# Optimization experiments

Measured on AMD Instinct MI355X. Metric: run time of the kernel, lower is better.

## Reference

```python
import jax, jax.numpy as jnp
import numpy as np

N_NODES = 50000
N_EDGES = 200000
D = 128
LN_EPS = 1e-5


def _layer_norm(x, g, b):
    mu = jnp.mean(x, axis=-1, keepdims=True)
    var = jnp.mean(jnp.square(x - mu), axis=-1, keepdims=True)
    return (x - mu) * jax.lax.rsqrt(var + LN_EPS) * g + b


def _mlp(x, W1, b1, W2, b2, W3, b3, g, beta):
    # 2 hidden ReLU layers + linear output + LayerNorm (MeshGraphNets style)
    h = jax.nn.relu(x @ W1 + b1)
    h = jax.nn.relu(h @ W2 + b2)
    h = h @ W3 + b3
    return _layer_norm(h, g, beta)


def setup_inputs() -> dict:
    key = jax.random.key(0)
    ks = jax.random.split(key, 12)
    d = {}
    d["node_features"] = jax.random.normal(ks[0], (N_NODES, D), dtype=jnp.float32)
    d["edge_features"] = jax.random.normal(ks[1], (N_EDGES, D), dtype=jnp.float32)
    d["senders"] = jax.random.randint(ks[2], (N_EDGES,), 0, N_NODES, dtype=jnp.int32)
    d["receivers"] = jax.random.randint(ks[3], (N_EDGES,), 0, N_NODES, dtype=jnp.int32)
    def lin(k, fan_in, fan_out):
        return jax.random.normal(k, (fan_in, fan_out), dtype=jnp.float32) / np.sqrt(fan_in)
    # edge MLP: [3D] -> D -> D -> D
    d["We1"] = lin(ks[4], 3 * D, D); d["be1"] = jnp.zeros((D,), jnp.float32)
    d["We2"] = lin(ks[5], D, D);     d["be2"] = jnp.zeros((D,), jnp.float32)
    d["We3"] = lin(ks[6], D, D);     d["be3"] = jnp.zeros((D,), jnp.float32)
    d["ge"] = jnp.ones((D,), jnp.float32); d["bege"] = jnp.zeros((D,), jnp.float32)
    # node MLP: [2D] -> D -> D -> D
    d["Wn1"] = lin(ks[7], 2 * D, D); d["bn1"] = jnp.zeros((D,), jnp.float32)
    d["Wn2"] = lin(ks[8], D, D);     d["bn2"] = jnp.zeros((D,), jnp.float32)
    d["Wn3"] = lin(ks[9], D, D);     d["bn3"] = jnp.zeros((D,), jnp.float32)
    d["gn"] = jnp.ones((D,), jnp.float32); d["begn"] = jnp.zeros((D,), jnp.float32)
    return d


def reference(node_features, edge_features, senders, receivers,
              We1, be1, We2, be2, We3, be3, ge, bege,
              Wn1, bn1, Wn2, bn2, Wn3, bn3, gn, begn):
    num_nodes = node_features.shape[0]
    # --- edge update: gather sender/receiver feats, concat, edge MLP ---
    edge_in = jnp.concatenate(
        [node_features[senders], node_features[receivers], edge_features], axis=-1)  # [E, 3D]
    new_edge = _mlp(edge_in, We1, be1, We2, be2, We3, be3, ge, bege)  # [E, D]
    # --- node update: scatter-sum aggregate, concat, node MLP ---
    agg = jax.ops.segment_sum(new_edge, receivers, num_segments=num_nodes)  # [N, D]
    node_in = jnp.concatenate([node_features, agg], axis=-1)  # [N, 2D]
    new_node = _mlp(node_in, Wn1, bn1, Wn2, bn2, Wn3, bn3, gn, begn)
    # --- residuals ---
    new_node = new_node + node_features
    new_edge = new_edge + edge_features
    return new_node, new_edge
```

## Files before the change

kernel.cpp:

```cpp
#include <hip/hip_runtime.h>

#define NNODES 50000
#define NEDGES 200000
#define DD 128
#define LN_EPS 1e-5f
#define NTH 256

typedef __attribute__((ext_vector_type(8))) short bf16x8;
typedef __attribute__((ext_vector_type(4))) float f32x4;
typedef __attribute__((ext_vector_type(16))) float f32x16;

template<int N> struct ic { static constexpr int value = N; };

__device__ __forceinline__ unsigned short bf_rne(float f) {
    union { float f; unsigned u; } v; v.f = f;
    return (unsigned short)((v.u + 0x7fffu + ((v.u >> 16) & 1u)) >> 16);
}

__device__ __forceinline__ void gload_lds16(const void* g, void* l) {
    __builtin_amdgcn_global_load_lds(
        (const __attribute__((address_space(1))) void*)g,
        (__attribute__((address_space(3))) void*)l, 16, 0, 0);
}

__global__ void build_wimg(const float* __restrict__ We1, const float* __restrict__ We2,
                           const float* __restrict__ We3, const float* __restrict__ Wn1,
                           const float* __restrict__ Wn2, const float* __restrict__ Wn3,
                           char* __restrict__ img_e, char* __restrict__ img_n) {
    int tid = blockIdx.x * NTH + threadIdx.x;
    const float* W; char* dst; int q;
    if      (tid <  6144) { W = We1; dst = img_e;             q = tid;         }
    else if (tid <  8192) { W = We2; dst = img_e + 12 * 8192; q = tid - 6144;  }
    else if (tid < 10240) { W = We3; dst = img_e + 16 * 8192; q = tid - 8192;  }
    else if (tid < 14336) { W = Wn1; dst = img_n;             q = tid - 10240; }
    else if (tid < 16384) { W = Wn2; dst = img_n + 8 * 8192;  q = tid - 14336; }
    else if (tid < 18432) { W = Wn3; dst = img_n + 12 * 8192; q = tid - 16384; }
    else return;
    int c = q >> 9, rem = q & 511;
    int ntile = rem >> 7, r2 = rem & 127, n32 = r2 >> 2, ks = r2 & 3;
    int n = ntile * 32 + n32;
    int sx = (n32 + (n32 >> 2)) & 3;
    int k0 = c * 32 + ks * 8;
    unsigned short o[8];
    #pragma unroll
    for (int e = 0; e < 8; ++e)
        o[e] = bf_rne(W[(size_t)(k0 + e) * DD + n]);
    uint4 val;
    val.x = (unsigned)o[0] | ((unsigned)o[1] << 16);
    val.y = (unsigned)o[2] | ((unsigned)o[3] << 16);
    val.z = (unsigned)o[4] | ((unsigned)o[5] << 16);
    val.w = (unsigned)o[6] | ((unsigned)o[7] << 16);
    *(uint4*)(dst + (size_t)c * 8192 + ntile * 2048 + n32 * 64 + ((ks ^ sx) << 4)) = val;
}

__global__ void csr_histo(const int* __restrict__ recv, int* __restrict__ cnt) {
    int e = blockIdx.x * NTH + threadIdx.x;
    if (e < NEDGES) atomicAdd(&cnt[recv[e]], 1);
}

__global__ __launch_bounds__(1024)
void csr_scan(const int* __restrict__ cnt, int* __restrict__ off, int* __restrict__ cursor) {
    __shared__ int part[1024];
    const int t = threadIdx.x;
    const int CH = (NNODES + 1023) / 1024;
    const int base = t * CH;
    int s = 0;
    for (int i = 0; i < CH; ++i) {
        int idx = base + i;
        if (idx < NNODES) s += cnt[idx];
    }
    part[t] = s;
    __syncthreads();
    for (int d = 1; d < 1024; d <<= 1) {
        int v = (t >= d) ? part[t - d] : 0;
        __syncthreads();
        part[t] += v;
        __syncthreads();
    }
    int run = (t == 0) ? 0 : part[t - 1];
    for (int i = 0; i < CH; ++i) {
        int idx = base + i;
        if (idx < NNODES) {
            off[idx] = run; cursor[idx] = run;
            run += cnt[idx];
        }
    }
    if (t == 1023) off[NNODES] = NEDGES;
}

__global__ void csr_fill(const int* __restrict__ recv, int* __restrict__ cursor,
                         int* __restrict__ elist) {
    int e = blockIdx.x * NTH + threadIdx.x;
    if (e < NEDGES) {
        int p = atomicAdd(&cursor[recv[e]], 1);
        elist[p] = e;
    }
}

__global__ __launch_bounds__(NTH)
void aggregate(const float* __restrict__ oute, const float* __restrict__ edgef,
               const int* __restrict__ off, const int* __restrict__ elist,
               float* __restrict__ agg) {
    const int n = blockIdx.x * 4 + (threadIdx.x >> 6);
    const int l = threadIdx.x & 63;
    if (n >= NNODES) return;
    const int j0 = off[n], j1 = off[n + 1];
    float ax = 0.f, ay = 0.f, bx = 0.f, by = 0.f;
    int j = j0;
    for (; j + 1 < j1; j += 2) {
        const int e0 = elist[j], e1 = elist[j + 1];
        const float2 o0 = ((const float2*)(oute  + (size_t)e0 * DD))[l];
        const float2 f0 = ((const float2*)(edgef + (size_t)e0 * DD))[l];
        const float2 o1 = ((const float2*)(oute  + (size_t)e1 * DD))[l];
        const float2 f1 = ((const float2*)(edgef + (size_t)e1 * DD))[l];
        ax += o0.x - f0.x; ay += o0.y - f0.y;
        bx += o1.x - f1.x; by += o1.y - f1.y;
    }
    if (j < j1) {
        const int e = elist[j];
        const float2 o  = ((const float2*)(oute  + (size_t)e * DD))[l];
        const float2 ef = ((const float2*)(edgef + (size_t)e * DD))[l];
        ax += o.x - ef.x; ay += o.y - ef.y;
    }
    float2 r; r.x = ax + bx; r.y = ay + by;
    ((float2*)(agg + (size_t)n * DD))[l] = r;
}

template<int MODE>
__global__ __launch_bounds__(NTH, 2)
void mgn_mfma(const float* __restrict__ nodef, const float* __restrict__ edgef,
              const int* __restrict__ senders, const int* __restrict__ receivers,
              const char* __restrict__ img,
              const float* __restrict__ b1, const float* __restrict__ b2,
              const float* __restrict__ b3,
              const float* __restrict__ gamma, const float* __restrict__ beta,
              const float* __restrict__ agg, float* __restrict__ outp)
{
    __shared__ char Wbuf[5 * 8192];
    __shared__ char Hb[4 * 8192];

    const int t  = threadIdx.x;
    const int w  = t >> 6;
    const int l  = t & 63;
    const int ln = l & 31;
    const int hi = l >> 5;
    const int row0 = blockIdx.x * 128;
    const int gm = row0 + w * 32 + ln;
    constexpr int NROWS = (MODE == 0) ? NEDGES : NNODES;
    constexpr int NK1   = (MODE == 0) ? 12 : 8;
    constexpr int NCH   = NK1 + 8;
    const int gmc = gm < NROWS ? gm : NROWS - 1;
    const int sxA = (ln + (ln >> 2)) & 3;
    const int sxH = ln & 15;

    int srow = 0, rrow = 0;
    if (MODE == 0) { srow = senders[gmc]; rrow = receivers[gmc]; }

    const f32x16 fz = {0.f,0.f,0.f,0.f,0.f,0.f,0.f,0.f,
                       0.f,0.f,0.f,0.f,0.f,0.f,0.f,0.f};
    f32x16 acc[4];
    #pragma unroll
    for (int nt = 0; nt < 4; ++nt) acc[nt] = fz;

    f32x4 barr[3][4];

    auto stageW = [&](int c) {
        const char* src = img + (size_t)c * 8192 + t * 16;
        char* dstl = Wbuf + (c % 5) * 8192 + t * 16;
        gload_lds16(src, dstl);
        gload_lds16(src + 4096, dstl + 4096);
    };

    auto loadBG = [&](int c, f32x4* dst) {
        const float* base;
        if (MODE == 0) {
            base = (c < 4) ? nodef + (size_t)srow * DD
                 : (c < 8) ? nodef + (size_t)rrow * DD
                           : edgef + (size_t)gmc * DD;
        } else {
            base = (c < 4) ? nodef + (size_t)gmc * DD
                           : agg   + (size_t)gmc * DD;
        }
        const float* p = base + (c & 3) * 32 + hi * 8;
        dst[0] = *(const f32x4*)p;
        dst[1] = *(const f32x4*)(p + 4);
        dst[2] = *(const f32x4*)(p + 16);
        dst[3] = *(const f32x4*)(p + 20);
    };

    auto cvtB = [&](const f32x4* br) {
        bf16x8 r;
        #pragma unroll
        for (int i = 0; i < 4; ++i) r[i]     = (short)bf_rne(br[0][i]);
        #pragma unroll
        for (int i = 0; i < 4; ++i) r[4 + i] = (short)bf_rne(br[1][i]);
        return r;
    };

    auto loadBH = [&](int ks, int kh) {
        const char* p = Hb + w * 8192 + ln * 256
                      + (((ks * 4 + kh * 2 + hi) ^ sxH) << 4);
        return *(const bf16x8*)p;
    };

    auto epiH = [&](const float* bias) {
        #pragma unroll
        for (int nt = 0; nt < 4; ++nt) {
            #pragma unroll
            for (int rq = 0; rq < 4; ++rq) {
                f32x4 bv = *(const f32x4*)(bias + nt * 32 + rq * 8 + hi * 4);
                unsigned short h[4];
                #pragma unroll
                for (int j = 0; j < 4; ++j)
                    h[j] = bf_rne(fmaxf(acc[nt][rq * 4 + j] + bv[j], 0.f));
                char* p = Hb + w * 8192 + ln * 256
                        + (((nt * 4 + rq) ^ sxH) << 4) + hi * 8;
                unsigned lo = (unsigned)h[0] | ((unsigned)h[1] << 16);
                unsigned hx = (unsigned)h[2] | ((unsigned)h[3] << 16);
                *(unsigned long long*)p =
                    (unsigned long long)lo | ((unsigned long long)hx << 32);
            }
            acc[nt] = fz;
        }
    };

    auto compute = [&](auto cc) {
        constexpr int c = decltype(cc)::value;
        const char* bp = Wbuf + (c % 5) * 8192 + ln * 64;
        #pragma unroll
        for (int kh = 0; kh < 2; ++kh) {
            bf16x8 b;
            if constexpr (c < NK1) b = cvtB(&barr[c % 3][kh * 2]);
            else                   b = loadBH((c - NK1) & 3, kh);
            #pragma unroll
            for (int nt = 0; nt < 4; ++nt) {
                bf16x8 a = *(const bf16x8*)(bp + nt * 2048
                            + (((kh * 2 + hi) ^ sxA) << 4));
                acc[nt] = __builtin_amdgcn_mfma_f32_32x32x16_bf16(a, b, acc[nt], 0, 0, 0);
            }
        }
    };

#define PITER(C, VM)                                                        \
    {                                                                       \
        if constexpr ((C) + 3 < NCH) stageW((C) + 3);                       \
        __builtin_amdgcn_sched_barrier(0);                                  \
        if constexpr ((C) + 2 < NK1) loadBG((C) + 2, barr[((C) + 2) % 3]);  \
        __builtin_amdgcn_sched_barrier(0);                                  \
        asm volatile("s_waitcnt vmcnt(" #VM ")" ::: "memory");              \
        __builtin_amdgcn_sched_barrier(0);                                  \
        __builtin_amdgcn_s_barrier();                                       \
        __builtin_amdgcn_sched_barrier(0);                                  \
        compute(ic<(C)>{});                                                 \
    }

    stageW(0);
    __builtin_amdgcn_sched_barrier(0);
    loadBG(0, barr[0]);
    __builtin_amdgcn_sched_barrier(0);
    stageW(1);
    __builtin_amdgcn_sched_barrier(0);
    loadBG(1, barr[1]);
    __builtin_amdgcn_sched_barrier(0);
    stageW(2);
    __builtin_amdgcn_sched_barrier(0);

    if constexpr (MODE == 0) {
        PITER(0, 18)  PITER(1, 18)  PITER(2, 18)  PITER(3, 22)  PITER(4, 22)
        PITER(5, 22)  PITER(6, 22)  PITER(7, 22)  PITER(8, 22)  PITER(9, 22)
        PITER(10, 18) PITER(11, 14)
        epiH(b1);
        PITER(12, 10) PITER(13, 6)  PITER(14, 6)  PITER(15, 6)
        epiH(b2);
        PITER(16, 6)  PITER(17, 4)  PITER(18, 2)  PITER(19, 0)
    } else {
        PITER(0, 18)  PITER(1, 18)  PITER(2, 18)  PITER(3, 22)  PITER(4, 22)
        PITER(5, 22)  PITER(6, 18)  PITER(7, 14)
        epiH(b1);
        PITER(8, 10)  PITER(9, 6)   PITER(10, 6)  PITER(11, 6)
        epiH(b2);
        PITER(12, 6)  PITER(13, 4)  PITER(14, 2)  PITER(15, 0)
    }
#undef PITER

    float vsum = 0.f, vsq = 0.f;
    #pragma unroll
    for (int nt = 0; nt < 4; ++nt) {
        #pragma unroll
        for (int rq = 0; rq < 4; ++rq) {
            f32x4 bv = *(const f32x4*)(b3 + nt * 32 + rq * 8 + hi * 4);
            #pragma unroll
            for (int j = 0; j < 4; ++j) {
                float v = acc[nt][rq * 4 + j] + bv[j];
                acc[nt][rq * 4 + j] = v;
                vsum += v; vsq += v * v;
            }
        }
    }
    vsum += __shfl_xor(vsum, 32);
    vsq  += __shfl_xor(vsq, 32);
    const float mu = vsum * (1.f / DD);
    const float rs = rsqrtf(vsq * (1.f / DD) - mu * mu + LN_EPS);

    if (gm < NROWS) {
        const float* resid = ((MODE == 0) ? edgef : nodef) + (size_t)gm * DD;
        #pragma unroll
        for (int nt = 0; nt < 4; ++nt) {
            #pragma unroll
            for (int rq = 0; rq < 4; ++rq) {
                const int n0 = nt * 32 + rq * 8 + hi * 4;
                f32x4 gv = *(const f32x4*)(gamma + n0);
                f32x4 bv = *(const f32x4*)(beta + n0);
                f32x4 rv = *(const f32x4*)(resid + n0);
                f32x4 o;
                #pragma unroll
                for (int j = 0; j < 4; ++j)
                    o[j] = (acc[nt][rq * 4 + j] - mu) * rs * gv[j] + bv[j] + rv[j];
                *(f32x4*)(outp + (size_t)gm * DD + n0) = o;
            }
        }
    }
}

extern "C" void kernel_launch(void* const* d_in, const int* in_sizes, int n_in,
                              void* d_out, int out_size, void* d_ws, size_t ws_size,
                              hipStream_t stream) {
    const float* nodef = (const float*)d_in[0];
    const float* edgef = (const float*)d_in[1];
    const int* senders   = (const int*)d_in[2];
    const int* receivers = (const int*)d_in[3];
    const float* We1 = (const float*)d_in[4],  *be1 = (const float*)d_in[5];
    const float* We2 = (const float*)d_in[6],  *be2 = (const float*)d_in[7];
    const float* We3 = (const float*)d_in[8],  *be3 = (const float*)d_in[9];
    const float* ge  = (const float*)d_in[10], *bege = (const float*)d_in[11];
    const float* Wn1 = (const float*)d_in[12], *bn1 = (const float*)d_in[13];
    const float* Wn2 = (const float*)d_in[14], *bn2 = (const float*)d_in[15];
    const float* Wn3 = (const float*)d_in[16], *bn3 = (const float*)d_in[17];
    const float* gn  = (const float*)d_in[18], *begn = (const float*)d_in[19];

    float* out_node = (float*)d_out;
    float* out_edge = (float*)d_out + (size_t)NNODES * DD;

    char* ws = (char*)d_ws;
    size_t o = 0;
    float* agg  = (float*)(ws + o); o += (size_t)NNODES * DD * 4;
    char* img_e = ws + o;           o += 20 * 8192;
    char* img_n = ws + o;           o += 16 * 8192;
    int* cnt    = (int*)(ws + o);   o += NNODES * 4;
    int* cursor = (int*)(ws + o);   o += NNODES * 4;
    int* off    = (int*)(ws + o);   o += (NNODES + 4) * 4;
    int* elist  = (int*)(ws + o);   o += NEDGES * 4;

    hipMemsetAsync(cnt, 0, NNODES * 4, stream);
    build_wimg<<<72, NTH, 0, stream>>>(We1, We2, We3, Wn1, Wn2, Wn3, img_e, img_n);

    const int egrid = (NEDGES + NTH - 1) / NTH;
    csr_histo<<<egrid, NTH, 0, stream>>>(receivers, cnt);
    csr_scan<<<1, 1024, 0, stream>>>(cnt, off, cursor);
    csr_fill<<<egrid, NTH, 0, stream>>>(receivers, cursor, elist);

    mgn_mfma<0><<<dim3((NEDGES + 127) / 128), dim3(NTH), 0, stream>>>(
        nodef, edgef, senders, receivers, img_e,
        be1, be2, be3, ge, bege, agg, out_edge);

    aggregate<<<(NNODES + 3) / 4, NTH, 0, stream>>>(out_edge, edgef, off, elist, agg);

    mgn_mfma<1><<<dim3((NNODES + 127) / 128), dim3(NTH), 0, stream>>>(
        nodef, edgef, senders, receivers, img_n,
        bn1, bn2, bn3, gn, begn, agg, out_node);
}
```

Baseline: 329.2 us.

## Load weights from global into registers, aggregate via bf16 edge buffer

Removes the LDS weight staging and barrier pipeline. Weight fragments are now read straight from global/L2 into registers with a register double buffer, which frees LDS so the kernel can declare 3 blocks per SM. The edge kernel also writes a bf16 copy of the pre-residual edge output. The aggregate kernel then reads half the bytes and no longer re-reads edge_features to subtract the residual, and the node kernel reads the aggregate directly as bf16. This trades more global/L2 weight traffic and extra bf16 rounding of the aggregate for less memory traffic in the aggregation and higher occupancy.

```diff
diff --git a/kernel.cpp b/kernel.cpp
--- a/kernel.cpp
+++ b/kernel.cpp
@@ -1,4 +1,5 @@
 #include <hip/hip_runtime.h>
+#include <hip/hip_bf16.h>
 
 #define NNODES 50000
 #define NEDGES 200000
@@ -12,15 +13,10 @@
 
 template<int N> struct ic { static constexpr int value = N; };
 
-__device__ __forceinline__ unsigned short bf_rne(float f) {
-    union { float f; unsigned u; } v; v.f = f;
-    return (unsigned short)((v.u + 0x7fffu + ((v.u >> 16) & 1u)) >> 16);
-}
-
-__device__ __forceinline__ void gload_lds16(const void* g, void* l) {
-    __builtin_amdgcn_global_load_lds(
-        (const __attribute__((address_space(1))) void*)g,
-        (__attribute__((address_space(3))) void*)l, 16, 0, 0);
+__device__ __forceinline__ unsigned short bfr(float f) {
+    union { __hip_bfloat16 b; unsigned short u; } v;
+    v.b = __float2bfloat16(f);
+    return v.u;
 }
 
 __global__ void build_wimg(const float* __restrict__ We1, const float* __restrict__ We2,
@@ -37,20 +33,19 @@
     else if (tid < 18432) { W = Wn3; dst = img_n + 12 * 8192; q = tid - 16384; }
     else return;
     int c = q >> 9, rem = q & 511;
-    int ntile = rem >> 7, r2 = rem & 127, n32 = r2 >> 2, ks = r2 & 3;
-    int n = ntile * 32 + n32;
-    int sx = (n32 + (n32 >> 2)) & 3;
+    int nt = rem >> 7, r2 = rem & 127, ks = r2 >> 5, n32 = r2 & 31;
+    int n = nt * 32 + n32;
     int k0 = c * 32 + ks * 8;
     unsigned short o[8];
     #pragma unroll
     for (int e = 0; e < 8; ++e)
-        o[e] = bf_rne(W[(size_t)(k0 + e) * DD + n]);
+        o[e] = bfr(W[(size_t)(k0 + e) * DD + n]);
     uint4 val;
     val.x = (unsigned)o[0] | ((unsigned)o[1] << 16);
     val.y = (unsigned)o[2] | ((unsigned)o[3] << 16);
     val.z = (unsigned)o[4] | ((unsigned)o[5] << 16);
     val.w = (unsigned)o[6] | ((unsigned)o[7] << 16);
-    *(uint4*)(dst + (size_t)c * 8192 + ntile * 2048 + n32 * 64 + ((ks ^ sx) << 4)) = val;
+    *(uint4*)(dst + (size_t)c * 8192 + nt * 2048 + ks * 512 + n32 * 16) = val;
 }
 
 __global__ void csr_histo(const int* __restrict__ recv, int* __restrict__ cnt) {
@@ -98,9 +93,9 @@
 }
 
 __global__ __launch_bounds__(NTH)
-void aggregate(const float* __restrict__ oute, const float* __restrict__ edgef,
+void aggregate(const unsigned* __restrict__ ybuf,
                const int* __restrict__ off, const int* __restrict__ elist,
-               float* __restrict__ agg) {
+               unsigned* __restrict__ aggb) {
     const int n = blockIdx.x * 4 + (threadIdx.x >> 6);
     const int l = threadIdx.x & 63;
     if (n >= NNODES) return;
@@ -108,35 +103,33 @@
     float ax = 0.f, ay = 0.f, bx = 0.f, by = 0.f;
     int j = j0;
     for (; j + 1 < j1; j += 2) {
-        const int e0 = elist[j], e1 = elist[j + 1];
-        const float2 o0 = ((const float2*)(oute  + (size_t)e0 * DD))[l];
-        const float2 f0 = ((const float2*)(edgef + (size_t)e0 * DD))[l];
-        const float2 o1 = ((const float2*)(oute  + (size_t)e1 * DD))[l];
-        const float2 f1 = ((const float2*)(edgef + (size_t)e1 * DD))[l];
-        ax += o0.x - f0.x; ay += o0.y - f0.y;
-        bx += o1.x - f1.x; by += o1.y - f1.y;
+        unsigned v0 = ybuf[(size_t)elist[j] * 64 + l];
+        unsigned v1 = ybuf[(size_t)elist[j + 1] * 64 + l];
+        ax += __uint_as_float(v0 << 16);
+        ay += __uint_as_float(v0 & 0xffff0000u);
+        bx += __uint_as_float(v1 << 16);
+        by += __uint_as_float(v1 & 0xffff0000u);
     }
     if (j < j1) {
-        const int e = elist[j];
-        const float2 o  = ((const float2*)(oute  + (size_t)e * DD))[l];
-        const float2 ef = ((const float2*)(edgef + (size_t)e * DD))[l];
-        ax += o.x - ef.x; ay += o.y - ef.y;
-    }
-    float2 r; r.x = ax + bx; r.y = ay + by;
-    ((float2*)(agg + (size_t)n * DD))[l] = r;
+        unsigned v = ybuf[(size_t)elist[j] * 64 + l];
+        ax += __uint_as_float(v << 16);
+        ay += __uint_as_float(v & 0xffff0000u);
+    }
+    float sx = ax + bx, sy = ay + by;
+    aggb[(size_t)n * 64 + l] = (unsigned)bfr(sx) | ((unsigned)bfr(sy) << 16);
 }
 
 template<int MODE>
-__global__ __launch_bounds__(NTH, 2)
+__global__ __launch_bounds__(NTH, 3)
 void mgn_mfma(const float* __restrict__ nodef, const float* __restrict__ edgef,
               const int* __restrict__ senders, const int* __restrict__ receivers,
               const char* __restrict__ img,
               const float* __restrict__ b1, const float* __restrict__ b2,
               const float* __restrict__ b3,
               const float* __restrict__ gamma, const float* __restrict__ beta,
-              const float* __restrict__ agg, float* __restrict__ outp)
+              const unsigned* __restrict__ aggb, unsigned* __restrict__ ybuf,
+              float* __restrict__ outp)
 {
-    __shared__ char Wbuf[5 * 8192];
     __shared__ char Hb[4 * 8192];
 
     const int t  = threadIdx.x;
@@ -150,7 +143,6 @@
     constexpr int NK1   = (MODE == 0) ? 12 : 8;
     constexpr int NCH   = NK1 + 8;
     const int gmc = gm < NROWS ? gm : NROWS - 1;
-    const int sxA = (ln + (ln >> 2)) & 3;
     const int sxH = ln & 15;
 
     int srow = 0, rrow = 0;
@@ -162,38 +154,46 @@
     #pragma unroll
     for (int nt = 0; nt < 4; ++nt) acc[nt] = fz;
 
-    f32x4 barr[3][4];
-
-    auto stageW = [&](int c) {
-        const char* src = img + (size_t)c * 8192 + t * 16;
-        char* dstl = Wbuf + (c % 5) * 8192 + t * 16;
-        gload_lds16(src, dstl);
-        gload_lds16(src + 4096, dstl + 4096);
-    };
-
-    auto loadBG = [&](int c, f32x4* dst) {
-        const float* base;
-        if (MODE == 0) {
-            base = (c < 4) ? nodef + (size_t)srow * DD
-                 : (c < 8) ? nodef + (size_t)rrow * DD
-                           : edgef + (size_t)gmc * DD;
+    bf16x8 aslot[2][4];
+    f32x4  bslot[2][4];
+
+    auto loadA = [&](int h, bf16x8* dst) {
+        const char* p = img + (size_t)(h >> 1) * 8192
+                      + (size_t)(((h & 1) * 2 + hi) * 512) + ln * 16;
+        #pragma unroll
+        for (int nt = 0; nt < 4; ++nt)
+            dst[nt] = *(const bf16x8*)(p + nt * 2048);
+    };
+
+    auto loadB = [&](auto CC, f32x4* dst) {
+        constexpr int c = decltype(CC)::value;
+        if constexpr (MODE == 1 && c >= 4) {
+            const char* p = (const char*)aggb + (size_t)gmc * 256 + (c & 3) * 64 + hi * 16;
+            dst[0] = *(const f32x4*)p;
+            dst[2] = *(const f32x4*)(p + 32);
         } else {
-            base = (c < 4) ? nodef + (size_t)gmc * DD
-                           : agg   + (size_t)gmc * DD;
-        }
-        const float* p = base + (c & 3) * 32 + hi * 8;
-        dst[0] = *(const f32x4*)p;
-        dst[1] = *(const f32x4*)(p + 4);
-        dst[2] = *(const f32x4*)(p + 16);
-        dst[3] = *(const f32x4*)(p + 20);
+            const float* base;
+            if constexpr (MODE == 0) {
+                base = (c < 4) ? nodef + (size_t)srow * DD
+                     : (c < 8) ? nodef + (size_t)rrow * DD
+                               : edgef + (size_t)gmc * DD;
+            } else {
+                base = nodef + (size_t)gmc * DD;
+            }
+            const float* p = base + (c & 3) * 32 + hi * 8;
+            dst[0] = *(const f32x4*)p;
+            dst[1] = *(const f32x4*)(p + 4);
+            dst[2] = *(const f32x4*)(p + 16);
+            dst[3] = *(const f32x4*)(p + 20);
+        }
     };
 
     auto cvtB = [&](const f32x4* br) {
         bf16x8 r;
         #pragma unroll
-        for (int i = 0; i < 4; ++i) r[i]     = (short)bf_rne(br[0][i]);
-        #pragma unroll
-        for (int i = 0; i < 4; ++i) r[4 + i] = (short)bf_rne(br[1][i]);
+        for (int i = 0; i < 4; ++i) r[i]     = (short)bfr(br[0][i]);
+        #pragma unroll
+        for (int i = 0; i < 4; ++i) r[4 + i] = (short)bfr(br[1][i]);
         return r;
     };
 
@@ -201,6 +201,19 @@
         const char* p = Hb + w * 8192 + ln * 256
                       + (((ks * 4 + kh * 2 + hi) ^ sxH) << 4);
         return *(const bf16x8*)p;
+    };
+
+    auto getB = [&](auto CC, int kh) -> bf16x8 {
+        constexpr int c = decltype(CC)::value;
+        if constexpr (c >= NK1) {
+            return loadBH((c - NK1) & 3, kh);
+        } else if constexpr (MODE == 1 && c >= 4) {
+            union { f32x4 f; bf16x8 h; } u;
+            u.f = bslot[c & 1][kh * 2];
+            return u.h;
+        } else {
+            return cvtB(&bslot[c & 1][kh * 2]);
+        }
     };
 
     auto epiH = [&](const float* bias) {
@@ -212,7 +225,7 @@
                 unsigned short h[4];
                 #pragma unroll
                 for (int j = 0; j < 4; ++j)
-                    h[j] = bf_rne(fmaxf(acc[nt][rq * 4 + j] + bv[j], 0.f));
+                    h[j] = bfr(fmaxf(acc[nt][rq * 4 + j] + bv[j], 0.f));
                 char* p = Hb + w * 8192 + ln * 256
                         + (((nt * 4 + rq) ^ sxH) << 4) + hi * 8;
                 unsigned lo = (unsigned)h[0] | ((unsigned)h[1] << 16);
@@ -224,64 +237,42 @@
         }
     };
 
-    auto compute = [&](auto cc) {
-        constexpr int c = decltype(cc)::value;
-        const char* bp = Wbuf + (c % 5) * 8192 + ln * 64;
-        #pragma unroll
-        for (int kh = 0; kh < 2; ++kh) {
-            bf16x8 b;
-            if constexpr (c < NK1) b = cvtB(&barr[c % 3][kh * 2]);
-            else                   b = loadBH((c - NK1) & 3, kh);
-            #pragma unroll
-            for (int nt = 0; nt < 4; ++nt) {
-                bf16x8 a = *(const bf16x8*)(bp + nt * 2048
-                            + (((kh * 2 + hi) ^ sxA) << 4));
-                acc[nt] = __builtin_amdgcn_mfma_f32_32x32x16_bf16(a, b, acc[nt], 0, 0, 0);
-            }
-        }
-    };
-
-#define PITER(C, VM)                                                        \
-    {                                                                       \
-        if constexpr ((C) + 3 < NCH) stageW((C) + 3);                       \
-        __builtin_amdgcn_sched_barrier(0);                                  \
-        if constexpr ((C) + 2 < NK1) loadBG((C) + 2, barr[((C) + 2) % 3]);  \
-        __builtin_amdgcn_sched_barrier(0);                                  \
-        asm volatile("s_waitcnt vmcnt(" #VM ")" ::: "memory");              \
-        __builtin_amdgcn_sched_barrier(0);                                  \
-        __builtin_amdgcn_s_barrier();                                       \
-        __builtin_amdgcn_sched_barrier(0);                                  \
-        compute(ic<(C)>{});                                                 \
-    }
-
-    stageW(0);
-    __builtin_amdgcn_sched_barrier(0);
-    loadBG(0, barr[0]);
-    __builtin_amdgcn_sched_barrier(0);
-    stageW(1);
-    __builtin_amdgcn_sched_barrier(0);
-    loadBG(1, barr[1]);
-    __builtin_amdgcn_sched_barrier(0);
-    stageW(2);
-    __builtin_amdgcn_sched_barrier(0);
-
-    if constexpr (MODE == 0) {
-        PITER(0, 18)  PITER(1, 18)  PITER(2, 18)  PITER(3, 22)  PITER(4, 22)
-        PITER(5, 22)  PITER(6, 22)  PITER(7, 22)  PITER(8, 22)  PITER(9, 22)
-        PITER(10, 18) PITER(11, 14)
-        epiH(b1);
-        PITER(12, 10) PITER(13, 6)  PITER(14, 6)  PITER(15, 6)
-        epiH(b2);
-        PITER(16, 6)  PITER(17, 4)  PITER(18, 2)  PITER(19, 0)
-    } else {
-        PITER(0, 18)  PITER(1, 18)  PITER(2, 18)  PITER(3, 22)  PITER(4, 22)
-        PITER(5, 22)  PITER(6, 18)  PITER(7, 14)
-        epiH(b1);
-        PITER(8, 10)  PITER(9, 6)   PITER(10, 6)  PITER(11, 6)
-        epiH(b2);
-        PITER(12, 6)  PITER(13, 4)  PITER(14, 2)  PITER(15, 0)
-    }
-#undef PITER
+    auto chunkfn = [&](auto CC) {
+        constexpr int c = decltype(CC)::value;
+        constexpr int h0 = 2 * c, h1 = 2 * c + 1;
+        loadA(h1, aslot[h1 & 1]);
+        {
+            bf16x8 b0 = getB(CC, 0);
+            #pragma unroll
+            for (int nt = 0; nt < 4; ++nt)
+                acc[nt] = __builtin_amdgcn_mfma_f32_32x32x16_bf16(
+                    aslot[h0 & 1][nt], b0, acc[nt], 0, 0, 0);
+        }
+        if constexpr (h1 + 1 < 2 * NCH) loadA(h1 + 1, aslot[(h1 + 1) & 1]);
+        {
+            bf16x8 b1 = getB(CC, 1);
+            #pragma unroll
+            for (int nt = 0; nt < 4; ++nt)
+                acc[nt] = __builtin_amdgcn_mfma_f32_32x32x16_bf16(
+                    aslot[h1 & 1][nt], b1, acc[nt], 0, 0, 0);
+        }
+        if constexpr (c + 2 < NK1) loadB(ic<c + 2>{}, bslot[c & 1]);
+    };
+
+    loadB(ic<0>{}, bslot[0]);
+    loadB(ic<1>{}, bslot[1]);
+    loadA(0, aslot[0]);
+
+#define CH(C)                                                                \
+    if constexpr ((C) < NCH) {                                               \
+        chunkfn(ic<(C)>{});                                                  \
+        if constexpr ((C) == NK1 - 1) epiH(b1);                              \
+        if constexpr ((C) == NK1 + 3) epiH(b2);                              \
+    }
+    CH(0)  CH(1)  CH(2)  CH(3)  CH(4)  CH(5)  CH(6)  CH(7)
+    CH(8)  CH(9)  CH(10) CH(11) CH(12) CH(13) CH(14) CH(15)
+    CH(16) CH(17) CH(18) CH(19)
+#undef CH
 
     float vsum = 0.f, vsq = 0.f;
     #pragma unroll
@@ -312,11 +303,20 @@
                 f32x4 gv = *(const f32x4*)(gamma + n0);
                 f32x4 bv = *(const f32x4*)(beta + n0);
                 f32x4 rv = *(const f32x4*)(resid + n0);
+                float y[4];
                 f32x4 o;
                 #pragma unroll
-                for (int j = 0; j < 4; ++j)
-                    o[j] = (acc[nt][rq * 4 + j] - mu) * rs * gv[j] + bv[j] + rv[j];
+                for (int j = 0; j < 4; ++j) {
+                    y[j] = (acc[nt][rq * 4 + j] - mu) * rs * gv[j] + bv[j];
+                    o[j] = y[j] + rv[j];
+                }
                 *(f32x4*)(outp + (size_t)gm * DD + n0) = o;
+                if (MODE == 0) {
+                    unsigned lo = (unsigned)bfr(y[0]) | ((unsigned)bfr(y[1]) << 16);
+                    unsigned hx = (unsigned)bfr(y[2]) | ((unsigned)bfr(y[3]) << 16);
+                    *(unsigned long long*)((char*)ybuf + (size_t)gm * 256 + n0 * 2) =
+                        (unsigned long long)lo | ((unsigned long long)hx << 32);
+                }
             }
         }
     }
@@ -343,7 +343,8 @@
 
     char* ws = (char*)d_ws;
     size_t o = 0;
-    float* agg  = (float*)(ws + o); o += (size_t)NNODES * DD * 4;
+    unsigned* aggb = (unsigned*)(ws + o); o += (size_t)NNODES * 256;
+    unsigned* ybuf = (unsigned*)(ws + o); o += (size_t)NEDGES * 256;
     char* img_e = ws + o;           o += 20 * 8192;
     char* img_n = ws + o;           o += 16 * 8192;
     int* cnt    = (int*)(ws + o);   o += NNODES * 4;
@@ -361,11 +362,11 @@
 
     mgn_mfma<0><<<dim3((NEDGES + 127) / 128), dim3(NTH), 0, stream>>>(
         nodef, edgef, senders, receivers, img_e,
-        be1, be2, be3, ge, bege, agg, out_edge);
-
-    aggregate<<<(NNODES + 3) / 4, NTH, 0, stream>>>(out_edge, edgef, off, elist, agg);
+        be1, be2, be3, ge, bege, aggb, ybuf, out_edge);
+
+    aggregate<<<(NNODES + 3) / 4, NTH, 0, stream>>>(ybuf, off, elist, aggb);
 
     mgn_mfma<1><<<dim3((NNODES + 127) / 128), dim3(NTH), 0, stream>>>(
         nodef, edgef, senders, receivers, img_n,
-        bn1, bn2, bn3, gn, begn, agg, out_node);
-}
+        bn1, bn2, bn3, gn, begn, aggb, ybuf, out_node);
+}
```

New measurement: 356.9 us. 8.4% more time.
